# Kernel optimization log

Measured on AMD Instinct MI355X. Metric: run time of the kernel, lower is better.

## Reference

```python
import jax, jax.numpy as jnp
import numpy as np

C = 128
H, W, Z = 128, 128, 16
N_CLASSES = 20


def conv3d(x, w, b, padding='SAME'):
    # x: [B,C,D,H,W], w: [O,I,kd,kh,kw]
    y = jax.lax.conv_general_dilated(x, w, (1, 1, 1), padding,
                                     dimension_numbers=('NCDHW', 'OIDHW', 'NCDHW'))
    return y + b[None, :, None, None, None]


def setup_inputs() -> dict:
    key = jax.random.key(0)
    ks = jax.random.split(key, 16)
    s = lambda fan: 1.0 / np.sqrt(fan)
    inp = {}
    inp['x3d'] = jax.random.normal(ks[0], (1, C, H, W, Z), jnp.float32)
    inp['prob_3d'] = jax.random.uniform(ks[1], (1, 1, H, W, Z), jnp.float32)
    # bottleneck Conv3d(C, C, k=3, pad=1)
    inp['w_bot'] = jax.random.normal(ks[2], (C, C, 3, 3, 3), jnp.float32) * s(C * 27)
    inp['b_bot'] = jnp.zeros((C,), jnp.float32)
    # occ_header: SDB(C -> C//2) approximated as conv3x3 + leaky_relu, then Conv3d(C//2, 2, k=3)
    inp['w_occ1'] = jax.random.normal(ks[3], (C // 2, C, 3, 3, 3), jnp.float32) * s(C * 27)
    inp['b_occ1'] = jnp.zeros((C // 2,), jnp.float32)
    inp['w_occ2'] = jax.random.normal(ks[4], (2, C // 2, 3, 3, 3), jnp.float32) * s(C // 2 * 27)
    inp['b_occ2'] = jnp.zeros((2,), jnp.float32)
    # mlp_prior: Linear(C, C//2) -> LayerNorm -> LeakyReLU -> Linear(C//2, C)
    inp['w_mlp1'] = jax.random.normal(ks[5], (C, C // 2), jnp.float32) * s(C)
    inp['b_mlp1'] = jnp.zeros((C // 2,), jnp.float32)
    inp['ln_g'] = jnp.ones((C // 2,), jnp.float32)
    inp['ln_b'] = jnp.zeros((C // 2,), jnp.float32)
    inp['w_mlp2'] = jax.random.normal(ks[6], (C // 2, C), jnp.float32) * s(C // 2)
    inp['b_mlp2'] = jnp.zeros((C,), jnp.float32)
    # sdb: Conv3d(C, C//2, k=3) + leaky_relu
    inp['w_sdb'] = jax.random.normal(ks[7], (C // 2, C, 3, 3, 3), jnp.float32) * s(C * 27)
    inp['b_sdb'] = jnp.zeros((C // 2,), jnp.float32)
    # ssc_header: Conv3d(C//2, n_classes, k=1)
    inp['w_ssc'] = jax.random.normal(ks[8], (N_CLASSES, C // 2, 1, 1, 1), jnp.float32) * s(C // 2)
    inp['b_ssc'] = jnp.zeros((N_CLASSES,), jnp.float32)
    return inp


def reference(x3d, prob_3d, w_bot, b_bot, w_occ1, b_occ1, w_occ2, b_occ2,
              w_mlp1, b_mlp1, ln_g, ln_b, w_mlp2, b_mlp2, w_sdb, b_sdb,
              w_ssc, b_ssc):
    # dense 3D bottleneck conv
    x = conv3d(x3d, w_bot, b_bot)  # [1,C,H,W,Z]
    # occupancy head on depth-reweighted features
    occ_in = x * prob_3d + x
    occ_h = jax.nn.leaky_relu(conv3d(occ_in, w_occ1, b_occ1))
    occ_logit = conv3d(occ_h, w_occ2, b_occ2)  # [1,2,H,W,Z]
    occ_prob = jax.nn.softmax(occ_logit, axis=1)[:, 1]  # [1,H,W,Z]
    occ_mask = (occ_prob > 0.5).reshape(-1)  # [N]

    # flatten voxel features: [N, C]
    x_flat = x[0].reshape(C, -1).T
    # prior MLP for non-occupied voxels (LayerNorm over feature dim)
    h = x_flat @ w_mlp1 + b_mlp1
    mu = jnp.mean(h, axis=-1, keepdims=True)
    var = jnp.var(h, axis=-1, keepdims=True)
    h = (h - mu) / jnp.sqrt(var + 1e-5) * ln_g + ln_b
    h = jax.nn.leaky_relu(h)
    prior = h @ w_mlp2 + b_mlp2  # [N, C]

    # gather/scatter fused as a masked select:
    # occupied voxels keep seed features, empty voxels take the prior
    vox_flat = jnp.where(occ_mask[:, None], x_flat, prior)  # [N, C]
    vox = vox_flat.T.reshape(1, C, H, W, Z)

    # SDB diffusion conv + SSC head
    d = jax.nn.leaky_relu(conv3d(vox, w_sdb, b_sdb))  # [1,C//2,H,W,Z]
    ssc_logit = conv3d(d, w_ssc, b_ssc)  # [1,20,H,W,Z]
    return ssc_logit
```

## Files before the change

kernel.cpp:

```cpp
#include <hip/hip_runtime.h>

#define AD 128
#define BDW 128
#define ZD 16
#define NVOX (AD*BDW*ZD)
#define SLAB 65536
#define NSLAB 4

typedef __attribute__((ext_vector_type(4))) float f32x4;
typedef __attribute__((ext_vector_type(8))) short bf16x8;
typedef __attribute__((ext_vector_type(8))) short s16x8;

__device__ __forceinline__ float leaky(float v) { return v > 0.f ? v : 0.01f * v; }

__device__ __forceinline__ f32x4 mfma16(bf16x8 a, bf16x8 b, f32x4 c) {
    return __builtin_amdgcn_mfma_f32_16x16x32_bf16(a, b, c, 0, 0, 0);
}

__device__ __forceinline__ void split3(float v, unsigned short& s1,
                                       unsigned short& s2, unsigned short& s3) {
    const unsigned u1 = __float_as_uint(v) & 0xFFFF0000u;
    const float r1 = v - __uint_as_float(u1);
    const unsigned u2 = __float_as_uint(r1) & 0xFFFF0000u;
    const float r2 = r1 - __uint_as_float(u2);
    s1 = (unsigned short)(u1 >> 16);
    s2 = (unsigned short)(u2 >> 16);
    s3 = (unsigned short)(__float_as_uint(r2) >> 16);
}

__device__ __forceinline__ int lds_a_off(int v, int chunk) {
    return ((v << 5) + (chunk << 3)) ^ ((v & 7) << 3);
}

__global__ __launch_bounds__(256) void wsplit3(const float* __restrict__ w,
                                               unsigned short* __restrict__ wp, int OC) {
    const int i = blockIdx.x * 256 + threadIdx.x;
    const int PS = OC * 3456;
    if (i >= PS) return;
    const int ko = i & 7;
    const int oc = (i >> 3) % OC;
    const int rest = (i >> 3) / OC;
    const int kc = rest & 3;
    const int kbt = rest >> 2;
    const int kb = kbt & 3, t = kbt >> 2;
    const int ic = kb * 32 + kc * 8 + ko;
    const float v = w[((size_t)oc * 128 + ic) * 27 + t];
    unsigned short s1, s2, s3;
    split3(v, s1, s2, s3);
    wp[i] = s1; wp[i + PS] = s2; wp[i + 2 * PS] = s3;
}

template<int OC, int PROD, int AQ, bool PREMUL, bool LEAKY, int RING, bool FUSESSC>
__global__ __launch_bounds__(AQ * 256, 1) void conv3s(const float* __restrict__ src,
                                              const float* __restrict__ prob,
                                              const unsigned short* __restrict__ W,
                                              const float* __restrict__ bias,
                                              float* __restrict__ out,
                                              const float* __restrict__ wssc,
                                              const float* __restrict__ bssc,
                                              int ablk_base) {
    constexpr int THREADS = AQ * 256;
    constexpr int NPL = (PROD == 6) ? 3 : 2;
    constexpr int HROWS = (AQ + 2) * 108;
    constexpr int PLH = HROWS * 32;
    constexpr int VOXT = AQ * 64;
    constexpr int NITEM = HROWS * 4;
    constexpr int PFI = (NITEM + THREADS - 1) / THREADS;
    constexpr int EPIH = OC * (VOXT + 1) * 2;
    constexpr int SMH = (NPL * PLH > EPIH) ? NPL * PLH : EPIH;
    __shared__ __align__(16) unsigned short smraw[SMH];
    unsigned short* sm0 = smraw;
    unsigned short* sm1 = smraw + PLH;
    unsigned short* sm2 = smraw + (NPL - 1) * PLH;

    const int tid = threadIdx.x;
    const int cpx = gridDim.x >> 3;
    const int bx = (blockIdx.x & 7) * cpx + (blockIdx.x >> 3);

    const int ablkA = ablk_base + (bx >> 5);
    const int b0    = (bx & 31) * 4;
    const int vbase = ablkA * (AQ * 2048) + b0 * 16;

    const int w = tid >> 6, l = tid & 63;
    const int lo16 = l & 15, hi4 = l >> 4;
    const int wo = w & 3, wm = w >> 2;
    constexpr int NF = OC / 64;
    constexpr int PS = OC * 3456;
    const int oc_off = wo * (16 * NF);

    f32x4 acc[4][NF];
    #pragma unroll
    for (int nf = 0; nf < NF; ++nf) {
        const float bv = bias[oc_off + nf * 16 + lo16];
        #pragma unroll
        for (int mf = 0; mf < 4; ++mf) acc[mf][nf] = f32x4{bv, bv, bv, bv};
    }

    float pf[PFI][8];
    float pfpm[PFI];

    #define PREFETCH(KB)                                                          \
        _Pragma("unroll")                                                         \
        for (int it = 0; it < PFI; ++it) {                                        \
            const int i = tid + it * THREADS;                                     \
            _Pragma("unroll")                                                     \
            for (int j = 0; j < 8; ++j) pf[it][j] = 0.f;                          \
            pfpm[it] = 1.f;                                                       \
            if (i < NITEM) {                                                      \
                const int q8 = i / HROWS;                                         \
                const int v  = i - q8 * HROWS;                                    \
                const int col = v / 18;                                           \
                const int zz  = v - col * 18;                                     \
                const int ha  = col / 6;                                          \
                const int hb  = col - ha * 6;                                     \
                const int a = ablkA * AQ + ha - 1;                                \
                const int b = b0 + hb - 1;                                        \
                const int z = zz - 1;                                             \
                if (((unsigned)a < 128u) && ((unsigned)b < 128u) &&               \
                    ((unsigned)z < 16u)) {                                        \
                    const int q = a * 2048 + b * 16 + z;                          \
                    const float* sp = src + (size_t)((KB) * 32 + q8 * 8) * NVOX + q; \
                    _Pragma("unroll")                                             \
                    for (int j = 0; j < 8; ++j) pf[it][j] = sp[(size_t)j * NVOX]; \
                    if (PREMUL) pfpm[it] = 1.f + prob[q];                         \
                }                                                                 \
            }                                                                     \
        }

    PREFETCH(0)

    #pragma unroll 1
    for (int kb = 0; kb < 4; ++kb) {
        __syncthreads();
        #pragma unroll
        for (int it = 0; it < PFI; ++it) {
            const int i = tid + it * THREADS;
            if (i < NITEM) {
                const int q8 = i / HROWS;
                const int v  = i - q8 * HROWS;
                s16x8 t1, t2, t3;
                #pragma unroll
                for (int j = 0; j < 8; ++j) {
                    float f = pf[it][j];
                    if (PREMUL) f *= pfpm[it];
                    unsigned short s1, s2, s3;
                    split3(f, s1, s2, s3);
                    t1[j] = (short)s1; t2[j] = (short)s2; t3[j] = (short)s3;
                }
                const int off = lds_a_off(v, q8);
                *(s16x8*)(sm0 + off) = t1;
                *(s16x8*)(sm1 + off) = t2;
                if (NPL == 3) *(s16x8*)(sm2 + off) = t3;
            }
        }
        if (kb < 3) PREFETCH(kb + 1)
        __syncthreads();

        #pragma unroll 1
        for (int ta = 0; ta < 3; ++ta) {
            #pragma unroll 1
            for (int tz = 0; tz < 3; ++tz) {
                bf16x8 A1[6], A2[6], A3[6];
                #pragma unroll
                for (int s = 0; s < 6; ++s) {
                    const int v = ((wm + ta) * 6 + s) * 18 + lo16 + tz;
                    const int ao = lds_a_off(v, hi4);
                    A1[s] = *(const bf16x8*)(sm0 + ao);
                    A2[s] = *(const bf16x8*)(sm1 + ao);
                    if (PROD == 6) A3[s] = *(const bf16x8*)(sm2 + ao);
                }
                #pragma unroll
                for (int tb = 0; tb < 3; ++tb) {
                    const int t = ta * 9 + tb * 3 + tz;
                    bf16x8 b1[NF], b2[NF], b3[NF];
                    #pragma unroll
                    for (int nf = 0; nf < NF; ++nf) {
                        const size_t wb = (((size_t)(t * 4 + kb) * 4 + hi4) * OC
                                           + oc_off + nf * 16 + lo16) * 8;
                        b1[nf] = *(const bf16x8*)(W + wb);
                        b2[nf] = *(const bf16x8*)(W + PS + wb);
                        if (PROD == 6) b3[nf] = *(const bf16x8*)(W + 2 * PS + wb);
                    }
                    #pragma unroll
                    for (int mf = 0; mf < 4; ++mf) {
                        const int s = mf + tb;
                        #pragma unroll
                        for (int nf = 0; nf < NF; ++nf) {
                            acc[mf][nf] = mfma16(A1[s], b1[nf], acc[mf][nf]);
                            acc[mf][nf] = mfma16(A1[s], b2[nf], acc[mf][nf]);
                            acc[mf][nf] = mfma16(A2[s], b1[nf], acc[mf][nf]);
                        }
                        if (PROD == 6) {
                            #pragma unroll
                            for (int nf = 0; nf < NF; ++nf) {
                                acc[mf][nf] = mfma16(A2[s], b2[nf], acc[mf][nf]);
                                acc[mf][nf] = mfma16(A1[s], b3[nf], acc[mf][nf]);
                                acc[mf][nf] = mfma16(A3[s], b1[nf], acc[mf][nf]);
                            }
                        }
                    }
                }
            }
        }
    }
    #undef PREFETCH

    __syncthreads();
    float* ldsT = (float*)smraw;
    #pragma unroll
    for (int mf = 0; mf < 4; ++mf)
        #pragma unroll
        for (int nf = 0; nf < NF; ++nf) {
            const int oc = oc_off + nf * 16 + lo16;
            #pragma unroll
            for (int r = 0; r < 4; ++r) {
                float vv = acc[mf][nf][r];
                if (LEAKY) vv = leaky(vv);
                ldsT[oc * (VOXT + 1) + wm * 64 + mf * 16 + hi4 * 4 + r] = vv;
            }
        }
    __syncthreads();
    if (FUSESSC) {
        for (int i = tid; i < 20 * VOXT; i += THREADS) {
            const int tv = i % VOXT;
            const int o = i / VOXT;
            float acc2 = bssc[o];
            #pragma unroll
            for (int ic = 0; ic < 64; ++ic)
                acc2 = fmaf(ldsT[ic * (VOXT + 1) + tv], wssc[o * 64 + ic], acc2);
            out[(size_t)o * NVOX + vbase + (tv >> 6) * 2048 + (tv & 63)] = acc2;
        }
    } else {
        int obase;
        if (RING == 0) obase = vbase;
        else           obase = ((vbase >> 16) % 3) * SLAB + (vbase & (SLAB - 1));
        const size_t outN = (RING == 0) ? (size_t)NVOX : (size_t)(3 * SLAB);
        for (int i = tid; i < OC * VOXT; i += THREADS) {
            const int oc = i / VOXT, tv = i % VOXT;
            out[(size_t)oc * outN + obase + (tv >> 6) * 2048 + (tv & 63)] =
                ldsT[oc * (VOXT + 1) + tv];
        }
    }
}

__global__ __launch_bounds__(256, 2) void occ2s(const float* __restrict__ HR,
                                                const float* __restrict__ w,
                                                const float* __restrict__ bias,
                                                unsigned char* __restrict__ mask,
                                                int s) {
    __shared__ float hl[324 * 36];
    __shared__ float wl[1728];
    __shared__ float red[4][66];

    const int tid = threadIdx.x;
    for (int i = tid; i < 1728; i += 256) wl[i] = w[1728 + i] - w[i];

    const int p0 = s * SLAB + blockIdx.x * 64;
    const int a0r = p0 >> 11;
    const int bb0 = (p0 >> 4) & 127;
    const int g = tid >> 6, v64 = tid & 63;

    float s0 = 0.f, s1 = 0.f;
    #pragma unroll 1
    for (int half = 0; half < 2; ++half) {
        __syncthreads();
        for (int i = tid; i < 2592; i += 256) {
            const int q4 = i / 324;
            const int v  = i - q4 * 324;
            const int col = v / 18;
            const int zz  = v - col * 18;
            const int ta  = col / 6;
            const int bi  = col - ta * 6;
            const int a = a0r + ta - 1;
            const int b = bb0 + bi - 1;
            const int z = zz - 1;
            f32x4 val = {0.f, 0.f, 0.f, 0.f};
            if (((unsigned)a < 128u) && ((unsigned)b < 128u) && ((unsigned)z < 16u)) {
                const int q = a * 2048 + b * 16 + z;
                const int rc = ((a >> 5) % 3) * SLAB + (q & (SLAB - 1));
                const int ic0 = half * 32 + q4 * 4;
                #pragma unroll
                for (int j = 0; j < 4; ++j)
                    val[j] = HR[(size_t)(ic0 + j) * (3 * SLAB) + rc];
            }
            *(f32x4*)(hl + v * 36 + q4 * 4) = val;
        }
        __syncthreads();
        #pragma unroll 1
        for (int t = 0; t < 27; ++t) {
            const int ta = t / 9, tb = (t / 3) % 3, tz = t % 3;
            const int vt = (ta * 6 + (v64 >> 4) + tb) * 18 + (v64 & 15) + tz;
            #pragma unroll
            for (int j = 0; j < 8; j += 2) {
                const int icl = g * 8 + j;
                const int ic = half * 32 + icl;
                s0 = fmaf(hl[vt * 36 + icl],     wl[ic * 27 + t],        s0);
                s1 = fmaf(hl[vt * 36 + icl + 1], wl[(ic + 1) * 27 + t],  s1);
            }
        }
    }
    red[g][v64] = s0 + s1;
    __syncthreads();
    if (g == 0) {
        float t0 = bias[1] - bias[0];
        #pragma unroll
        for (int k = 0; k < 4; ++k) t0 += red[k][v64];
        mask[p0 + v64] = (t0 > 0.f) ? 1 : 0;
    }
}

__global__ __launch_bounds__(256) void mlp_vox(float* __restrict__ x,
                                               const float* __restrict__ w1,
                                               const float* __restrict__ b1,
                                               const float* __restrict__ g,
                                               const float* __restrict__ beta,
                                               const float* __restrict__ w2,
                                               const float* __restrict__ b2,
                                               const unsigned char* __restrict__ mask) {
    const int p = blockIdx.x * 256 + threadIdx.x;
    float h[64];
    #pragma unroll
    for (int j = 0; j < 64; ++j) h[j] = b1[j];
    #pragma unroll 1
    for (int c = 0; c < 128; ++c) {
        const float xv = x[(size_t)c * NVOX + p];
        #pragma unroll
        for (int j = 0; j < 64; ++j) h[j] = fmaf(xv, w1[c * 64 + j], h[j]);
    }
    float mu = 0.f;
    #pragma unroll
    for (int j = 0; j < 64; ++j) mu += h[j];
    mu *= (1.f / 64.f);
    float var = 0.f;
    #pragma unroll
    for (int j = 0; j < 64; ++j) { const float d = h[j] - mu; var = fmaf(d, d, var); }
    var *= (1.f / 64.f);
    const float rs = rsqrtf(var + 1e-5f);
    #pragma unroll
    for (int j = 0; j < 64; ++j) h[j] = leaky((h[j] - mu) * rs * g[j] + beta[j]);

    const bool m = mask[p] != 0;
    #pragma unroll 1
    for (int c = 0; c < 128; ++c) {
        float pr = b2[c];
        #pragma unroll
        for (int j = 0; j < 64; ++j) pr = fmaf(h[j], w2[j * 128 + c], pr);
        const size_t idx = (size_t)c * NVOX + p;
        x[idx] = m ? x[idx] : pr;
    }
}

extern "C" void kernel_launch(void* const* d_in, const int* in_sizes, int n_in,
                              void* d_out, int out_size, void* d_ws, size_t ws_size,
                              hipStream_t stream) {
    const float* x3d    = (const float*)d_in[0];
    const float* prob   = (const float*)d_in[1];
    const float* w_bot  = (const float*)d_in[2];
    const float* b_bot  = (const float*)d_in[3];
    const float* w_occ1 = (const float*)d_in[4];
    const float* b_occ1 = (const float*)d_in[5];
    const float* w_occ2 = (const float*)d_in[6];
    const float* b_occ2 = (const float*)d_in[7];
    const float* w_mlp1 = (const float*)d_in[8];
    const float* b_mlp1 = (const float*)d_in[9];
    const float* ln_g   = (const float*)d_in[10];
    const float* ln_b   = (const float*)d_in[11];
    const float* w_mlp2 = (const float*)d_in[12];
    const float* b_mlp2 = (const float*)d_in[13];
    const float* w_sdb  = (const float*)d_in[14];
    const float* b_sdb  = (const float*)d_in[15];
    const float* w_ssc  = (const float*)d_in[16];
    const float* b_ssc  = (const float*)d_in[17];

    char* ws = (char*)d_ws;
    float* X32 = (float*)(ws);
    float* HR  = (float*)(ws + 134217728);
    unsigned short* WB3 = (unsigned short*)(ws + 184549376);
    unsigned short* W13 = (unsigned short*)(ws + 187203584);
    unsigned short* WS3 = (unsigned short*)(ws + 188530688);
    unsigned char* mask = (unsigned char*)(ws + 189857792);

    const dim3 blk(256);
    const dim3 blk10(1024);

    wsplit3<<<1728, blk, 0, stream>>>(w_bot,  WB3, 128);
    wsplit3<<<864,  blk, 0, stream>>>(w_occ1, W13, 64);
    wsplit3<<<864,  blk, 0, stream>>>(w_sdb,  WS3, 64);

    conv3s<128, 6, 4, false, false, 0, false><<<1024, blk10, 0, stream>>>(
        x3d, nullptr, WB3, b_bot, X32, nullptr, nullptr, 0);

    for (int s = 0; s < NSLAB; ++s) {
        conv3s<64, 6, 4, true, true, 2, false><<<256, blk10, 0, stream>>>(
            X32, prob, W13, b_occ1, HR, nullptr, nullptr, 8 * s);
        if (s >= 1) occ2s<<<1024, blk, 0, stream>>>(HR, w_occ2, b_occ2, mask, s - 1);
    }
    occ2s<<<1024, blk, 0, stream>>>(HR, w_occ2, b_occ2, mask, NSLAB - 1);

    mlp_vox<<<1024, blk, 0, stream>>>(X32, w_mlp1, b_mlp1, ln_g, ln_b, w_mlp2, b_mlp2, mask);

    conv3s<64, 3, 4, false, true, 0, true><<<1024, blk10, 0, stream>>>(
        X32, nullptr, WS3, b_sdb, (float*)d_out, w_ssc, b_ssc, 0);
}
```

Baseline: 2.244 ms.

## Pre-split conv inputs into packed bf16 planes in global memory

Adds a presplit kernel that converts fp32 activations (optionally premultiplied by 1+prob) into three packed bf16 split planes with 8 channels interleaved per voxel. The conv kernels then load ready-made 16-byte vectors instead of 8 strided fp32 loads plus per-block split arithmetic. The MLP kernel also writes its output straight into this plane layout for the final conv. This removes redundant split work on halo data and the strided fp32 gathers, at the cost of extra full-volume passes and a much larger workspace. A fallback to the old path is kept for when the workspace is too small.

```diff
diff --git a/kernel.cpp b/kernel.cpp
--- a/kernel.cpp
+++ b/kernel.cpp
@@ -6,6 +6,7 @@
 #define NVOX (AD*BDW*ZD)
 #define SLAB 65536
 #define NSLAB 4
+#define PL1H ((size_t)16 * NVOX * 8)
 
 typedef __attribute__((ext_vector_type(4))) float f32x4;
 typedef __attribute__((ext_vector_type(8))) short bf16x8;
@@ -50,8 +51,30 @@
     wp[i] = s1; wp[i + PS] = s2; wp[i + 2 * PS] = s3;
 }
 
-template<int OC, int PROD, int AQ, bool PREMUL, bool LEAKY, int RING, bool FUSESSC>
-__global__ __launch_bounds__(AQ * 256, 1) void conv3s(const float* __restrict__ src,
+__global__ __launch_bounds__(256) void presplit(const float* __restrict__ src,
+                                                const float* __restrict__ prob,
+                                                unsigned short* __restrict__ P) {
+    const int i = blockIdx.x * 256 + threadIdx.x;
+    const int q8 = i >> 18;
+    const int q  = i & (NVOX - 1);
+    const float pm = prob ? (1.f + prob[q]) : 1.f;
+    s16x8 t1, t2, t3;
+    #pragma unroll
+    for (int j = 0; j < 8; ++j) {
+        const float v = src[(size_t)(q8 * 8 + j) * NVOX + q] * pm;
+        unsigned short s1, s2, s3;
+        split3(v, s1, s2, s3);
+        t1[j] = (short)s1; t2[j] = (short)s2; t3[j] = (short)s3;
+    }
+    unsigned short* pp = P + ((size_t)q8 * NVOX + q) * 8;
+    *(s16x8*)pp = t1;
+    *(s16x8*)(pp + PL1H) = t2;
+    *(s16x8*)(pp + 2 * PL1H) = t3;
+}
+
+template<int OC, int PROD, int AQ, bool PLANES, bool PREMUL, bool LEAKY,
+         int RING, bool FUSESSC>
+__global__ __launch_bounds__(AQ * 256, 1) void conv3s(const void* __restrict__ srcv,
                                               const float* __restrict__ prob,
                                               const unsigned short* __restrict__ W,
                                               const float* __restrict__ bias,
@@ -73,6 +96,9 @@
     unsigned short* sm1 = smraw + PLH;
     unsigned short* sm2 = smraw + (NPL - 1) * PLH;
 
+    const float* src = (const float*)srcv;
+    const unsigned short* SP = (const unsigned short*)srcv;
+
     const int tid = threadIdx.x;
     const int cpx = gridDim.x >> 3;
     const int bx = (blockIdx.x & 7) * cpx + (blockIdx.x >> 3);
@@ -98,14 +124,21 @@
 
     float pf[PFI][8];
     float pfpm[PFI];
+    s16x8 pt1[PFI], pt2[PFI], pt3[PFI];
+    const s16x8 z8 = {0, 0, 0, 0, 0, 0, 0, 0};
 
     #define PREFETCH(KB)                                                          \
         _Pragma("unroll")                                                         \
         for (int it = 0; it < PFI; ++it) {                                        \
             const int i = tid + it * THREADS;                                     \
-            _Pragma("unroll")                                                     \
-            for (int j = 0; j < 8; ++j) pf[it][j] = 0.f;                          \
-            pfpm[it] = 1.f;                                                       \
+            if constexpr (PLANES) {                                               \
+                pt1[it] = z8; pt2[it] = z8;                                       \
+                if (NPL == 3) pt3[it] = z8;                                       \
+            } else {                                                              \
+                _Pragma("unroll")                                                 \
+                for (int j = 0; j < 8; ++j) pf[it][j] = 0.f;                      \
+                pfpm[it] = 1.f;                                                   \
+            }                                                                     \
             if (i < NITEM) {                                                      \
                 const int q8 = i / HROWS;                                         \
                 const int v  = i - q8 * HROWS;                                    \
@@ -119,10 +152,18 @@
                 if (((unsigned)a < 128u) && ((unsigned)b < 128u) &&               \
                     ((unsigned)z < 16u)) {                                        \
                     const int q = a * 2048 + b * 16 + z;                          \
-                    const float* sp = src + (size_t)((KB) * 32 + q8 * 8) * NVOX + q; \
-                    _Pragma("unroll")                                             \
-                    for (int j = 0; j < 8; ++j) pf[it][j] = sp[(size_t)j * NVOX]; \
-                    if (PREMUL) pfpm[it] = 1.f + prob[q];                         \
+                    if constexpr (PLANES) {                                       \
+                        const unsigned short* pp =                                \
+                            SP + ((size_t)((KB) * 4 + q8) * NVOX + q) * 8;        \
+                        pt1[it] = *(const s16x8*)pp;                              \
+                        pt2[it] = *(const s16x8*)(pp + PL1H);                     \
+                        if (NPL == 3) pt3[it] = *(const s16x8*)(pp + 2 * PL1H);   \
+                    } else {                                                      \
+                        const float* sp = src + (size_t)((KB) * 32 + q8 * 8) * NVOX + q; \
+                        _Pragma("unroll")                                         \
+                        for (int j = 0; j < 8; ++j) pf[it][j] = sp[(size_t)j * NVOX]; \
+                        if (PREMUL) pfpm[it] = 1.f + prob[q];                     \
+                    }                                                             \
                 }                                                                 \
             }                                                                     \
         }
@@ -139,13 +180,18 @@
                 const int q8 = i / HROWS;
                 const int v  = i - q8 * HROWS;
                 s16x8 t1, t2, t3;
-                #pragma unroll
-                for (int j = 0; j < 8; ++j) {
-                    float f = pf[it][j];
-                    if (PREMUL) f *= pfpm[it];
-                    unsigned short s1, s2, s3;
-                    split3(f, s1, s2, s3);
-                    t1[j] = (short)s1; t2[j] = (short)s2; t3[j] = (short)s3;
+                if constexpr (PLANES) {
+                    t1 = pt1[it]; t2 = pt2[it];
+                    if (NPL == 3) t3 = pt3[it];
+                } else {
+                    #pragma unroll
+                    for (int j = 0; j < 8; ++j) {
+                        float f = pf[it][j];
+                        if (PREMUL) f *= pfpm[it];
+                        unsigned short s1, s2, s3;
+                        split3(f, s1, s2, s3);
+                        t1[j] = (short)s1; t2[j] = (short)s2; t3[j] = (short)s3;
+                    }
                 }
                 const int off = lds_a_off(v, q8);
                 *(s16x8*)(sm0 + off) = t1;
@@ -309,7 +355,9 @@
     }
 }
 
+template<bool PLANES>
 __global__ __launch_bounds__(256) void mlp_vox(float* __restrict__ x,
+                                               unsigned short* __restrict__ P,
                                                const float* __restrict__ w1,
                                                const float* __restrict__ b1,
                                                const float* __restrict__ g,
@@ -340,13 +388,35 @@
     for (int j = 0; j < 64; ++j) h[j] = leaky((h[j] - mu) * rs * g[j] + beta[j]);
 
     const bool m = mask[p] != 0;
-    #pragma unroll 1
-    for (int c = 0; c < 128; ++c) {
-        float pr = b2[c];
-        #pragma unroll
-        for (int j = 0; j < 64; ++j) pr = fmaf(h[j], w2[j * 128 + c], pr);
-        const size_t idx = (size_t)c * NVOX + p;
-        x[idx] = m ? x[idx] : pr;
+    if constexpr (PLANES) {
+        #pragma unroll 1
+        for (int c8 = 0; c8 < 16; ++c8) {
+            s16x8 t1, t2;
+            #pragma unroll
+            for (int cc = 0; cc < 8; ++cc) {
+                const int c = c8 * 8 + cc;
+                float pr = b2[c];
+                #pragma unroll
+                for (int j = 0; j < 64; ++j) pr = fmaf(h[j], w2[j * 128 + c], pr);
+                const float xv = x[(size_t)c * NVOX + p];
+                const float res = m ? xv : pr;
+                unsigned short s1, s2, s3;
+                split3(res, s1, s2, s3);
+                t1[cc] = (short)s1; t2[cc] = (short)s2;
+            }
+            unsigned short* pp = P + ((size_t)c8 * NVOX + p) * 8;
+            *(s16x8*)pp = t1;
+            *(s16x8*)(pp + PL1H) = t2;
+        }
+    } else {
+        #pragma unroll 1
+        for (int c = 0; c < 128; ++c) {
+            float pr = b2[c];
+            #pragma unroll
+            for (int j = 0; j < 64; ++j) pr = fmaf(h[j], w2[j * 128 + c], pr);
+            const size_t idx = (size_t)c * NVOX + p;
+            x[idx] = m ? x[idx] : pr;
+        }
     }
 }
 
@@ -372,33 +442,68 @@
     const float* w_ssc  = (const float*)d_in[16];
     const float* b_ssc  = (const float*)d_in[17];
 
-    char* ws = (char*)d_ws;
-    float* X32 = (float*)(ws);
-    float* HR  = (float*)(ws + 134217728);
-    unsigned short* WB3 = (unsigned short*)(ws + 184549376);
-    unsigned short* W13 = (unsigned short*)(ws + 187203584);
-    unsigned short* WS3 = (unsigned short*)(ws + 188530688);
-    unsigned char* mask = (unsigned char*)(ws + 189857792);
-
     const dim3 blk(256);
     const dim3 blk10(1024);
-
-    wsplit3<<<1728, blk, 0, stream>>>(w_bot,  WB3, 128);
-    wsplit3<<<864,  blk, 0, stream>>>(w_occ1, W13, 64);
-    wsplit3<<<864,  blk, 0, stream>>>(w_sdb,  WS3, 64);
-
-    conv3s<128, 6, 4, false, false, 0, false><<<1024, blk10, 0, stream>>>(
-        x3d, nullptr, WB3, b_bot, X32, nullptr, nullptr, 0);
-
-    for (int s = 0; s < NSLAB; ++s) {
-        conv3s<64, 6, 4, true, true, 2, false><<<256, blk10, 0, stream>>>(
-            X32, prob, W13, b_occ1, HR, nullptr, nullptr, 8 * s);
-        if (s >= 1) occ2s<<<1024, blk, 0, stream>>>(HR, w_occ2, b_occ2, mask, s - 1);
-    }
-    occ2s<<<1024, blk, 0, stream>>>(HR, w_occ2, b_occ2, mask, NSLAB - 1);
-
-    mlp_vox<<<1024, blk, 0, stream>>>(X32, w_mlp1, b_mlp1, ln_g, ln_b, w_mlp2, b_mlp2, mask);
-
-    conv3s<64, 3, 4, false, true, 0, true><<<1024, blk10, 0, stream>>>(
-        X32, nullptr, WS3, b_sdb, (float*)d_out, w_ssc, b_ssc, 0);
-}
+    char* ws = (char*)d_ws;
+
+    const size_t NEED_PLANES = 391446528ULL;
+
+    if (ws_size >= NEED_PLANES) {
+        unsigned short* P = (unsigned short*)(ws);
+        float* X32 = (float*)(ws + 201326592);
+        float* HR  = (float*)(ws + 335544320);
+        unsigned short* WB3 = (unsigned short*)(ws + 385875968);
+        unsigned short* W13 = (unsigned short*)(ws + 388530176);
+        unsigned short* WS3 = (unsigned short*)(ws + 389857280);
+        unsigned char* mask = (unsigned char*)(ws + 391184384);
+
+        wsplit3<<<1728, blk, 0, stream>>>(w_bot,  WB3, 128);
+        wsplit3<<<864,  blk, 0, stream>>>(w_occ1, W13, 64);
+        wsplit3<<<864,  blk, 0, stream>>>(w_sdb,  WS3, 64);
+
+        presplit<<<16384, blk, 0, stream>>>(x3d, nullptr, P);
+        conv3s<128, 6, 4, true, false, false, 0, false><<<1024, blk10, 0, stream>>>(
+            P, nullptr, WB3, b_bot, X32, nullptr, nullptr, 0);
+
+        presplit<<<16384, blk, 0, stream>>>(X32, prob, P);
+        for (int s = 0; s < NSLAB; ++s) {
+            conv3s<64, 6, 4, true, false, true, 2, false><<<256, blk10, 0, stream>>>(
+                P, nullptr, W13, b_occ1, HR, nullptr, nullptr, 8 * s);
+            if (s >= 1) occ2s<<<1024, blk, 0, stream>>>(HR, w_occ2, b_occ2, mask, s - 1);
+        }
+        occ2s<<<1024, blk, 0, stream>>>(HR, w_occ2, b_occ2, mask, NSLAB - 1);
+
+        mlp_vox<true><<<1024, blk, 0, stream>>>(X32, P, w_mlp1, b_mlp1, ln_g, ln_b,
+                                                w_mlp2, b_mlp2, mask);
+
+        conv3s<64, 3, 4, true, false, true, 0, true><<<1024, blk10, 0, stream>>>(
+            P, nullptr, WS3, b_sdb, (float*)d_out, w_ssc, b_ssc, 0);
+    } else {
+        float* X32 = (float*)(ws);
+        float* HR  = (float*)(ws + 134217728);
+        unsigned short* WB3 = (unsigned short*)(ws + 184549376);
+        unsigned short* W13 = (unsigned short*)(ws + 187203584);
+        unsigned short* WS3 = (unsigned short*)(ws + 188530688);
+        unsigned char* mask = (unsigned char*)(ws + 189857792);
+
+        wsplit3<<<1728, blk, 0, stream>>>(w_bot,  WB3, 128);
+        wsplit3<<<864,  blk, 0, stream>>>(w_occ1, W13, 64);
+        wsplit3<<<864,  blk, 0, stream>>>(w_sdb,  WS3, 64);
+
+        conv3s<128, 6, 4, false, false, false, 0, false><<<1024, blk10, 0, stream>>>(
+            x3d, nullptr, WB3, b_bot, X32, nullptr, nullptr, 0);
+
+        for (int s = 0; s < NSLAB; ++s) {
+            conv3s<64, 6, 4, false, true, true, 2, false><<<256, blk10, 0, stream>>>(
+                X32, prob, W13, b_occ1, HR, nullptr, nullptr, 8 * s);
+            if (s >= 1) occ2s<<<1024, blk, 0, stream>>>(HR, w_occ2, b_occ2, mask, s - 1);
+        }
+        occ2s<<<1024, blk, 0, stream>>>(HR, w_occ2, b_occ2, mask, NSLAB - 1);
+
+        mlp_vox<false><<<1024, blk, 0, stream>>>(X32, nullptr, w_mlp1, b_mlp1, ln_g,
+                                                 ln_b, w_mlp2, b_mlp2, mask);
+
+        conv3s<64, 3, 4, false, false, true, 0, true><<<1024, blk10, 0, stream>>>(
+            X32, nullptr, WS3, b_sdb, (float*)d_out, w_ssc, b_ssc, 0);
+    }
+}
```

Result: slower. 2.590 ms (+15.4%).

## Fuse occ2 head into occ1 conv launches as extra blocks with 4-slot ring

Applied to the files above, without the earlier changes.

The separate occ2s kernel launches are removed. Their work runs as extra 1024-thread blocks appended to the occ1 conv grid, so the occupancy head for earlier slabs runs alongside the occ1 conv of later slabs and overlaps with it. The HR ring buffer grows from 3 to 4 slabs so in-flight slabs are not overwritten, and the three weight-split kernels are merged into one launch. The cost is more workspace, occ2 blocks running at 1024 threads with the conv's large LDS allocation, and a tail launch that only does occ2 work.

```diff
diff --git a/kernel.cpp b/kernel.cpp
--- a/kernel.cpp
+++ b/kernel.cpp
@@ -6,6 +6,7 @@
 #define NVOX (AD*BDW*ZD)
 #define SLAB 65536
 #define NSLAB 4
+#define NRING 4
 
 typedef __attribute__((ext_vector_type(4))) float f32x4;
 typedef __attribute__((ext_vector_type(8))) short bf16x8;
@@ -32,9 +33,18 @@
     return ((v << 5) + (chunk << 3)) ^ ((v & 7) << 3);
 }
 
-__global__ __launch_bounds__(256) void wsplit3(const float* __restrict__ w,
-                                               unsigned short* __restrict__ wp, int OC) {
-    const int i = blockIdx.x * 256 + threadIdx.x;
+__global__ __launch_bounds__(256) void wsplit_all(const float* __restrict__ wb,
+                                                  const float* __restrict__ wo,
+                                                  const float* __restrict__ wsd,
+                                                  unsigned short* __restrict__ WB,
+                                                  unsigned short* __restrict__ WO,
+                                                  unsigned short* __restrict__ WS) {
+    int blk = blockIdx.x;
+    const float* src; unsigned short* dst; int OC;
+    if (blk < 1728)      { src = wb;  dst = WB; OC = 128; }
+    else if (blk < 2592) { src = wo;  dst = WO; OC = 64; blk -= 1728; }
+    else                 { src = wsd; dst = WS; OC = 64; blk -= 2592; }
+    const int i = blk * 256 + threadIdx.x;
     const int PS = OC * 3456;
     if (i >= PS) return;
     const int ko = i & 7;
@@ -44,13 +54,85 @@
     const int kbt = rest >> 2;
     const int kb = kbt & 3, t = kbt >> 2;
     const int ic = kb * 32 + kc * 8 + ko;
-    const float v = w[((size_t)oc * 128 + ic) * 27 + t];
+    const float v = src[((size_t)oc * 128 + ic) * 27 + t];
     unsigned short s1, s2, s3;
     split3(v, s1, s2, s3);
-    wp[i] = s1; wp[i + PS] = s2; wp[i + 2 * PS] = s3;
-}
-
-template<int OC, int PROD, int AQ, bool PREMUL, bool LEAKY, int RING, bool FUSESSC>
+    dst[i] = s1; dst[i + PS] = s2; dst[i + 2 * PS] = s3;
+}
+
+__device__ void occ2_role(const float* __restrict__ HR,
+                          const float* __restrict__ w,
+                          const float* __restrict__ b,
+                          unsigned char* __restrict__ mask,
+                          int bx2raw, int sp_base, unsigned short* smraw) {
+    const int grp = bx2raw >> 8;
+    const int r   = bx2raw & 255;
+    const int bx  = (r & 7) * 32 + (r >> 3);
+    const int sp  = sp_base + grp;
+
+    float* hl  = (float*)smraw;
+    float* wl  = hl + 648 * 36;
+    float* red = wl + 1728;
+
+    const int tid = threadIdx.x;
+    for (int i = tid; i < 1728; i += 1024) wl[i] = w[1728 + i] - w[i];
+
+    const int a0 = sp * 32 + (bx >> 5) * 4;
+    const int b0 = (bx & 31) * 4;
+    const int g = tid >> 8, v = tid & 255;
+    const int a_l = v >> 6, b_l = (v >> 4) & 3, z = v & 15;
+
+    float acc0 = 0.f, acc1 = 0.f;
+    #pragma unroll 1
+    for (int half = 0; half < 2; ++half) {
+        __syncthreads();
+        for (int i = tid; i < 5184; i += 1024) {
+            const int q4 = i / 648;
+            const int hv = i - q4 * 648;
+            const int col = hv / 18;
+            const int zz  = hv - col * 18;
+            const int ha  = col / 6;
+            const int hb  = col - ha * 6;
+            const int a = a0 + ha - 1;
+            const int bb = b0 + hb - 1;
+            const int zq = zz - 1;
+            f32x4 val = {0.f, 0.f, 0.f, 0.f};
+            if (((unsigned)a < 128u) && ((unsigned)bb < 128u) && ((unsigned)zq < 16u)) {
+                const int q = a * 2048 + bb * 16 + zq;
+                const int rc = ((a >> 5) & (NRING - 1)) * SLAB + (q & (SLAB - 1));
+                const int ic0 = half * 32 + q4 * 4;
+                #pragma unroll
+                for (int j = 0; j < 4; ++j)
+                    val[j] = HR[(size_t)(ic0 + j) * (NRING * SLAB) + rc];
+            }
+            *(f32x4*)(hl + hv * 36 + q4 * 4) = val;
+        }
+        __syncthreads();
+        #pragma unroll 1
+        for (int t = 0; t < 27; ++t) {
+            const int ta = t / 9, tb = (t / 3) % 3, tz = t % 3;
+            const int vt = ((a_l + ta) * 6 + b_l + tb) * 18 + z + tz;
+            #pragma unroll
+            for (int j = 0; j < 8; j += 2) {
+                const int icl = g * 8 + j;
+                const int ic = half * 32 + icl;
+                acc0 = fmaf(hl[vt * 36 + icl],     wl[ic * 27 + t],       acc0);
+                acc1 = fmaf(hl[vt * 36 + icl + 1], wl[(ic + 1) * 27 + t], acc1);
+            }
+        }
+    }
+    red[g * 260 + v] = acc0 + acc1;
+    __syncthreads();
+    if (g == 0) {
+        float t0 = b[1] - b[0];
+        #pragma unroll
+        for (int k = 0; k < 4; ++k) t0 += red[k * 260 + v];
+        mask[(a0 + a_l) * 2048 + (b0 + b_l) * 16 + z] = (t0 > 0.f) ? 1 : 0;
+    }
+}
+
+template<int OC, int PROD, int AQ, bool PREMUL, bool LEAKY, int RING,
+         bool FUSESSC, bool FUSEOCC2>
 __global__ __launch_bounds__(AQ * 256, 1) void conv3s(const float* __restrict__ src,
                                               const float* __restrict__ prob,
                                               const unsigned short* __restrict__ W,
@@ -58,6 +140,8 @@
                                               float* __restrict__ out,
                                               const float* __restrict__ wssc,
                                               const float* __restrict__ bssc,
+                                              unsigned char* __restrict__ maskp,
+                                              int occ1_grid, int sp_base,
                                               int ablk_base) {
     constexpr int THREADS = AQ * 256;
     constexpr int NPL = (PROD == 6) ? 3 : 2;
@@ -73,9 +157,16 @@
     unsigned short* sm1 = smraw + PLH;
     unsigned short* sm2 = smraw + (NPL - 1) * PLH;
 
+    if (FUSEOCC2 && (int)blockIdx.x >= occ1_grid) {
+        occ2_role(out, wssc, bssc, maskp, (int)blockIdx.x - occ1_grid,
+                  sp_base, smraw);
+        return;
+    }
+
     const int tid = threadIdx.x;
-    const int cpx = gridDim.x >> 3;
-    const int bx = (blockIdx.x & 7) * cpx + (blockIdx.x >> 3);
+    const int cg = FUSEOCC2 ? occ1_grid : (int)gridDim.x;
+    const int cpx = cg >> 3;
+    const int bx = ((int)blockIdx.x & 7) * cpx + ((int)blockIdx.x >> 3);
 
     const int ablkA = ablk_base + (bx >> 5);
     const int b0    = (bx & 31) * 4;
@@ -233,79 +324,13 @@
     } else {
         int obase;
         if (RING == 0) obase = vbase;
-        else           obase = ((vbase >> 16) % 3) * SLAB + (vbase & (SLAB - 1));
-        const size_t outN = (RING == 0) ? (size_t)NVOX : (size_t)(3 * SLAB);
+        else           obase = ((vbase >> 16) & (NRING - 1)) * SLAB + (vbase & (SLAB - 1));
+        const size_t outN = (RING == 0) ? (size_t)NVOX : (size_t)(NRING * SLAB);
         for (int i = tid; i < OC * VOXT; i += THREADS) {
             const int oc = i / VOXT, tv = i % VOXT;
             out[(size_t)oc * outN + obase + (tv >> 6) * 2048 + (tv & 63)] =
                 ldsT[oc * (VOXT + 1) + tv];
         }
-    }
-}
-
-__global__ __launch_bounds__(256, 2) void occ2s(const float* __restrict__ HR,
-                                                const float* __restrict__ w,
-                                                const float* __restrict__ bias,
-                                                unsigned char* __restrict__ mask,
-                                                int s) {
-    __shared__ float hl[324 * 36];
-    __shared__ float wl[1728];
-    __shared__ float red[4][66];
-
-    const int tid = threadIdx.x;
-    for (int i = tid; i < 1728; i += 256) wl[i] = w[1728 + i] - w[i];
-
-    const int p0 = s * SLAB + blockIdx.x * 64;
-    const int a0r = p0 >> 11;
-    const int bb0 = (p0 >> 4) & 127;
-    const int g = tid >> 6, v64 = tid & 63;
-
-    float s0 = 0.f, s1 = 0.f;
-    #pragma unroll 1
-    for (int half = 0; half < 2; ++half) {
-        __syncthreads();
-        for (int i = tid; i < 2592; i += 256) {
-            const int q4 = i / 324;
-            const int v  = i - q4 * 324;
-            const int col = v / 18;
-            const int zz  = v - col * 18;
-            const int ta  = col / 6;
-            const int bi  = col - ta * 6;
-            const int a = a0r + ta - 1;
-            const int b = bb0 + bi - 1;
-            const int z = zz - 1;
-            f32x4 val = {0.f, 0.f, 0.f, 0.f};
-            if (((unsigned)a < 128u) && ((unsigned)b < 128u) && ((unsigned)z < 16u)) {
-                const int q = a * 2048 + b * 16 + z;
-                const int rc = ((a >> 5) % 3) * SLAB + (q & (SLAB - 1));
-                const int ic0 = half * 32 + q4 * 4;
-                #pragma unroll
-                for (int j = 0; j < 4; ++j)
-                    val[j] = HR[(size_t)(ic0 + j) * (3 * SLAB) + rc];
-            }
-            *(f32x4*)(hl + v * 36 + q4 * 4) = val;
-        }
-        __syncthreads();
-        #pragma unroll 1
-        for (int t = 0; t < 27; ++t) {
-            const int ta = t / 9, tb = (t / 3) % 3, tz = t % 3;
-            const int vt = (ta * 6 + (v64 >> 4) + tb) * 18 + (v64 & 15) + tz;
-            #pragma unroll
-            for (int j = 0; j < 8; j += 2) {
-                const int icl = g * 8 + j;
-                const int ic = half * 32 + icl;
-                s0 = fmaf(hl[vt * 36 + icl],     wl[ic * 27 + t],        s0);
-                s1 = fmaf(hl[vt * 36 + icl + 1], wl[(ic + 1) * 27 + t],  s1);
-            }
-        }
-    }
-    red[g][v64] = s0 + s1;
-    __syncthreads();
-    if (g == 0) {
-        float t0 = bias[1] - bias[0];
-        #pragma unroll
-        for (int k = 0; k < 4; ++k) t0 += red[k][v64];
-        mask[p0 + v64] = (t0 > 0.f) ? 1 : 0;
     }
 }
 
@@ -375,30 +400,29 @@
     char* ws = (char*)d_ws;
     float* X32 = (float*)(ws);
     float* HR  = (float*)(ws + 134217728);
-    unsigned short* WB3 = (unsigned short*)(ws + 184549376);
-    unsigned short* W13 = (unsigned short*)(ws + 187203584);
-    unsigned short* WS3 = (unsigned short*)(ws + 188530688);
-    unsigned char* mask = (unsigned char*)(ws + 189857792);
+    unsigned short* WB3 = (unsigned short*)(ws + 201326592);
+    unsigned short* W13 = (unsigned short*)(ws + 203980800);
+    unsigned short* WS3 = (unsigned short*)(ws + 205307904);
+    unsigned char* mask = (unsigned char*)(ws + 206635008);
 
     const dim3 blk(256);
     const dim3 blk10(1024);
 
-    wsplit3<<<1728, blk, 0, stream>>>(w_bot,  WB3, 128);
-    wsplit3<<<864,  blk, 0, stream>>>(w_occ1, W13, 64);
-    wsplit3<<<864,  blk, 0, stream>>>(w_sdb,  WS3, 64);
-
-    conv3s<128, 6, 4, false, false, 0, false><<<1024, blk10, 0, stream>>>(
-        x3d, nullptr, WB3, b_bot, X32, nullptr, nullptr, 0);
+    wsplit_all<<<3456, blk, 0, stream>>>(w_bot, w_occ1, w_sdb, WB3, W13, WS3);
+
+    conv3s<128, 6, 4, false, false, 0, false, false><<<1024, blk10, 0, stream>>>(
+        x3d, nullptr, WB3, b_bot, X32, nullptr, nullptr, nullptr, 0, 0, 0);
 
     for (int s = 0; s < NSLAB; ++s) {
-        conv3s<64, 6, 4, true, true, 2, false><<<256, blk10, 0, stream>>>(
-            X32, prob, W13, b_occ1, HR, nullptr, nullptr, 8 * s);
-        if (s >= 1) occ2s<<<1024, blk, 0, stream>>>(HR, w_occ2, b_occ2, mask, s - 1);
-    }
-    occ2s<<<1024, blk, 0, stream>>>(HR, w_occ2, b_occ2, mask, NSLAB - 1);
+        const int grid = (s >= 2) ? 512 : 256;
+        conv3s<64, 6, 4, true, true, 2, false, true><<<grid, blk10, 0, stream>>>(
+            X32, prob, W13, b_occ1, HR, w_occ2, b_occ2, mask, 256, s - 2, 8 * s);
+    }
+    conv3s<64, 6, 4, true, true, 2, false, true><<<512, blk10, 0, stream>>>(
+        X32, prob, W13, b_occ1, HR, w_occ2, b_occ2, mask, 0, 2, 0);
 
     mlp_vox<<<1024, blk, 0, stream>>>(X32, w_mlp1, b_mlp1, ln_g, ln_b, w_mlp2, b_mlp2, mask);
 
-    conv3s<64, 3, 4, false, true, 0, true><<<1024, blk10, 0, stream>>>(
-        X32, nullptr, WS3, b_sdb, (float*)d_out, w_ssc, b_ssc, 0);
-}
+    conv3s<64, 3, 4, false, true, 0, true, false><<<1024, blk10, 0, stream>>>(
+        X32, nullptr, WS3, b_sdb, (float*)d_out, w_ssc, b_ssc, nullptr, 0, 0, 0);
+}
```

New measurement: 2.171 ms, median of 2. 1.03x faster.
